# Performance work log

Hardware: AMD Instinct MI355X
Metric: run time of the kernel (lower is better)

Reference implementation:

```python
import jax, jax.numpy as jnp
import numpy as np

D = 128           # embed_dim
NUM_LAYERS = 2
N_CLASSES = 4
OUT_CELL = 64
SPEAKERS = 2
INPUT_DIMS = [768, 74, 35]
B, T = 32, 60


def setup_inputs() -> dict:
    key = jax.random.key(0)
    ks = jax.random.split(key, 24)
    inp = {}
    inp['x0'] = jax.random.normal(ks[0], (B, T, INPUT_DIMS[0]), jnp.float32)
    inp['x1'] = jax.random.normal(ks[1], (B, T, INPUT_DIMS[1]), jnp.float32)
    inp['x2'] = jax.random.normal(ks[2], (B, T, INPUT_DIMS[2]), jnp.float32)
    inp['smask'] = jax.random.normal(ks[3], (B, T, SPEAKERS), jnp.float32)  # argmax -> speaker ids
    # modality projections
    for i, d in enumerate(INPUT_DIMS):
        inp[f'Wp{i}'] = jax.random.normal(ks[4 + i], (d, D), jnp.float32) / np.float32(np.sqrt(d))
        inp[f'bp{i}'] = jnp.zeros((D,), jnp.float32)
    # shared PositionEmbedding (ModuleList([m]*3) shares params)
    inp['freq_emb'] = jax.random.normal(ks[7], (SPEAKERS, D), jnp.float32) * 0.1
    inp['phase_emb'] = jax.random.normal(ks[8], (SPEAKERS, D), jnp.float32)
    # shared QRNNCell (ModuleList([cell]*num_layers) shares params)
    inp['U_x'] = jnp.linalg.qr(jax.random.normal(ks[9], (D, D), jnp.float32))[0]
    inp['U_h'] = jnp.linalg.qr(jax.random.normal(ks[10], (D, D), jnp.float32))[0]
    inp['Lambda'] = jnp.float32(0.5)
    # QMeasurement kernel (real/imag parts of D measurement vectors)
    inp['kernel_r'] = jnp.eye(D, dtype=jnp.float32) + 0.05 * jax.random.normal(ks[11], (D, D), jnp.float32)
    inp['kernel_i'] = 0.05 * jax.random.normal(ks[12], (D, D), jnp.float32)
    # SimpleNet fc_out
    inp['W1'] = jax.random.normal(ks[13], (D, OUT_CELL), jnp.float32) / np.float32(np.sqrt(D))
    inp['b1'] = jnp.zeros((OUT_CELL,), jnp.float32)
    inp['W2'] = jax.random.normal(ks[14], (OUT_CELL, N_CLASSES), jnp.float32) / np.float32(np.sqrt(OUT_CELL))
    inp['b2'] = jnp.zeros((N_CLASSES,), jnp.float32)
    return inp


def _qmn_forward(x0, x1, x2, smask, Wp0, bp0, Wp1, bp1, Wp2, bp2,
                 freq_emb, phase_emb, U_x, U_h, Lambda,
                 kernel_r, kernel_i, W1, b1, W2, b2):
    xs = [x0, x1, x2]
    Ws = [(Wp0, bp0), (Wp1, bp1), (Wp2, bp2)]
    reps = [jax.nn.relu(x @ W + b) for x, (W, b) in zip(xs, Ws)]           # [B,T,D] each
    # mixture weights: softmax over per-modality L2 norms
    norms = jnp.concatenate([jnp.linalg.norm(r, axis=-1, keepdims=True) for r in reps], axis=-1)
    weights = jax.nn.softmax(norms, axis=-1)                               # [B,T,M]
    # shared phase embedding: phase = t * freq[speaker] + phase[speaker]
    ids = jnp.argmax(smask, axis=-1)                                       # [B,T] int
    pos = jnp.arange(T, dtype=jnp.float32)[None, :, None]                  # [1,T,1]
    phase = pos * freq_emb[ids] + phase_emb[ids]                           # [B,T,D]
    cosp, sinp = jnp.cos(phase), jnp.sin(phase)
    # mixed density matrices rho = sum_m w_m |v_m><v_m|
    rho_r = jnp.zeros((B, T, D, D), jnp.float32)
    rho_i = jnp.zeros((B, T, D, D), jnp.float32)
    for m, r in enumerate(reps):
        a = r / jnp.maximum(jnp.linalg.norm(r, axis=-1, keepdims=True), 1e-12)
        pr = a * cosp                                                       # real amplitude
        pi = a * sinp                                                       # imag amplitude
        w = weights[..., m][..., None, None]
        rho_r = rho_r + w * (jnp.einsum('btm,btn->btmn', pr, pr) + jnp.einsum('btm,btn->btmn', pi, pi))
        rho_i = rho_i + w * (jnp.einsum('btm,btn->btmn', pi, pr) - jnp.einsum('btm,btn->btmn', pr, pi))
    # time-major for scan
    sr = jnp.transpose(rho_r, (1, 0, 2, 3))                                # [T,B,D,D]
    si = jnp.transpose(rho_i, (1, 0, 2, 3))

    def cell(h, x):
        hr, hi = h
        xr, xi = x
        Xr = jnp.einsum('mp,bpq,nq->bmn', U_x, xr, U_x)
        Xi = jnp.einsum('mp,bpq,nq->bmn', U_x, xi, U_x)
        Hr = jnp.einsum('mp,bpq,nq->bmn', U_h, hr, U_h)
        Hi = jnp.einsum('mp,bpq,nq->bmn', U_h, hi, U_h)
        nr = Lambda * Hr + (1.0 - Lambda) * Xr
        ni = Lambda * Hi + (1.0 - Lambda) * Xi
        return (nr, ni), (nr, ni)

    h0 = (jnp.broadcast_to(jnp.eye(D, dtype=jnp.float32) / D, (B, D, D)),
          jnp.zeros((B, D, D), jnp.float32))
    for _ in range(NUM_LAYERS):  # same shared cell params each layer
        _, (sr, si) = jax.lax.scan(cell, h0, (sr, si))
    # QMeasurement: p_k = Re(v_k^dag rho v_k), unit-norm complex measurement vectors
    nrm = jnp.sqrt(jnp.sum(kernel_r**2 + kernel_i**2, axis=1, keepdims=True))
    vr = kernel_r / jnp.maximum(nrm, 1e-12)                                # [K,D], K=D
    vi = kernel_i / jnp.maximum(nrm, 1e-12)
    probs = (jnp.einsum('tbmn,km,kn->tbk', sr, vr, vr)
             + jnp.einsum('tbmn,km,kn->tbk', sr, vi, vi)
             - jnp.einsum('tbmn,km,kn->tbk', si, vr, vi)
             + jnp.einsum('tbmn,km,kn->tbk', si, vi, vr))                  # [T,B,D]
    # SimpleNet (dropout = identity at inference)
    hid = jax.nn.relu(probs @ W1 + b1)
    out = jnp.tanh(hid @ W2 + b2)                                          # [T,B,C]
    out = jnp.transpose(out, (1, 0, 2))                                    # [B,T,C]
    return jax.nn.log_softmax(out, axis=2)


def reference(x0, x1, x2, smask, Wp0, bp0, Wp1, bp1, Wp2, bp2,
              freq_emb, phase_emb, U_x, U_h, Lambda,
              kernel_r, kernel_i, W1, b1, W2, b2):
    return _qmn_forward(x0, x1, x2, smask, Wp0, bp0, Wp1, bp1, Wp2, bp2,
                        freq_emb, phase_emb, U_x, U_h, Lambda,
                        kernel_r, kernel_i, W1, b1, W2, b2)
```

## Files before the change

kernel.cpp:

```cpp
#include <hip/hip_runtime.h>


#define DB 32
#define DT 60
#define DD 128
#define BT (DB*DT)
#define SP 136

typedef unsigned short ushort_t;
typedef __attribute__((ext_vector_type(8))) __bf16 bf16x8;
typedef __attribute__((ext_vector_type(8))) unsigned short ushort8_t;
typedef __attribute__((ext_vector_type(4))) float  float4v;

__device__ __forceinline__ float bf2f(ushort_t u){
  union { unsigned int i; float f; } x; x.i = ((unsigned int)u) << 16; return x.f;
}
__device__ __forceinline__ ushort_t f2bf(float f){
  union { float f; unsigned int i; } x; x.f = f;
  unsigned int lsb = (x.i >> 16) & 1u;
  return (ushort_t)((x.i + 0x7FFFu + lsb) >> 16);
}
__device__ __forceinline__ unsigned int f2bfpk(float a, float b){
#if defined(__gfx950__) && __has_builtin(__builtin_amdgcn_cvt_pk_bf16_f32)
  auto v = __builtin_amdgcn_cvt_pk_bf16_f32(a, b);
  unsigned int r; __builtin_memcpy(&r, &v, 4); return r;
#else
  return (unsigned int)f2bf(a) | ((unsigned int)f2bf(b) << 16);
#endif
}
__device__ __forceinline__ void split2(float v, ushort_t& h, ushort_t& l){
  h = f2bf(v); l = f2bf(v - bf2f(h));
}

template<int RT, int CT, bool ALO, bool BLO>
__device__ __forceinline__ void gemm_t(const ushort_t* Ah, const ushort_t* Al,
                                       const ushort_t* Bh, const ushort_t* Bl,
                                       float4v* acc, int row0, int col0, int gma, int q)
{
  for (int ks = 0; ks < 4; ks++){
    int ko = ks*32 + q*8;
    bf16x8 aF[RT], aL[RT], bF[CT], bL[CT];
    #pragma unroll
    for (int R = 0; R < RT; R++){
      int row = row0 + 16*R + gma;
      aF[R] = *(const bf16x8*)&Ah[row*SP + ko];
      if (ALO) aL[R] = *(const bf16x8*)&Al[row*SP + ko];
    }
    #pragma unroll
    for (int C = 0; C < CT; C++){
      int row = col0 + 16*C + gma;
      bF[C] = *(const bf16x8*)&Bh[row*SP + ko];
      if (BLO) bL[C] = *(const bf16x8*)&Bl[row*SP + ko];
    }
    #pragma unroll
    for (int R = 0; R < RT; R++)
      #pragma unroll
      for (int C = 0; C < CT; C++){
        float4v c = acc[R*CT+C];
        c = __builtin_amdgcn_mfma_f32_16x16x32_bf16(aF[R], bF[C], c, 0, 0, 0);
        if (BLO) c = __builtin_amdgcn_mfma_f32_16x16x32_bf16(aF[R], bL[C], c, 0, 0, 0);
        if (ALO) c = __builtin_amdgcn_mfma_f32_16x16x32_bf16(aL[R], bF[C], c, 0, 0, 0);
        acc[R*CT+C] = c;
      }
  }
}

template<int RT, int CT>
__device__ __forceinline__ void emit_t(const float4v* acc, ushort_t* dst, int stride,
                                       int row0, int col0, int gma, int q){
  #pragma unroll
  for (int R = 0; R < RT; R++)
    #pragma unroll
    for (int C = 0; C < CT; C++){
      int c = col0 + 16*C + gma, r0 = row0 + 16*R + 4*q;
      uint2 o;
      o.x = f2bfpk(acc[R*CT+C][0], acc[R*CT+C][1]);
      o.y = f2bfpk(acc[R*CT+C][2], acc[R*CT+C][3]);
      *(uint2*)&dst[(size_t)c*stride + r0] = o;
    }
}
template<int RT, int CT>
__device__ __forceinline__ void emit_split_t(const float4v* acc, ushort_t* dh, ushort_t* dl, int stride,
                                             int row0, int col0, int gma, int q){
  #pragma unroll
  for (int R = 0; R < RT; R++)
    #pragma unroll
    for (int C = 0; C < CT; C++){
      int c = col0 + 16*C + gma, r0 = row0 + 16*R + 4*q;
      ushort4 hh, ll;
      split2(acc[R*CT+C][0], hh.x, ll.x); split2(acc[R*CT+C][1], hh.y, ll.y);
      split2(acc[R*CT+C][2], hh.z, ll.z); split2(acc[R*CT+C][3], hh.w, ll.w);
      *(ushort4*)&dh[(size_t)c*stride + r0] = hh;
      *(ushort4*)&dl[(size_t)c*stride + r0] = ll;
    }
}
template<int NT>
__device__ __forceinline__ void lds_load_mat(ushort_t* dst, const ushort_t* src, int tid){
  for (int i = tid*8; i < 16384; i += NT*8){
    int r = i >> 7, k = i & 127;
    *(ushort8_t*)&dst[r*SP + k] = *(const ushort8_t*)&src[i];
  }
}
template<int NT>
__device__ __forceinline__ void lds_load_rows16(ushort_t* dst, const ushort_t* src, int tid){
  for (int i = tid*8; i < 2048; i += NT*8){
    int r = i >> 7, k = i & 127;
    *(ushort8_t*)&dst[r*SP + k] = *(const ushort8_t*)&src[i];
  }
}
template<int NT>
__device__ __forceinline__ void lds_load_mat2(ushort_t* d0, const ushort_t* s0,
                                              ushort_t* d1, const ushort_t* s1, int tid){
  constexpr int CH = 16384/(NT*8);
  ushort8_t r0[CH], r1[CH];
  #pragma unroll
  for (int c = 0; c < CH; c++) r0[c] = *(const ushort8_t*)&s0[tid*8 + c*NT*8];
  #pragma unroll
  for (int c = 0; c < CH; c++) r1[c] = *(const ushort8_t*)&s1[tid*8 + c*NT*8];
  #pragma unroll
  for (int c = 0; c < CH; c++){
    int i = tid*8 + c*NT*8; int r = i >> 7, k = i & 127;
    *(ushort8_t*)&d0[r*SP + k] = r0[c];
  }
  #pragma unroll
  for (int c = 0; c < CH; c++){
    int i = tid*8 + c*NT*8; int r = i >> 7, k = i & 127;
    *(ushort8_t*)&d1[r*SP + k] = r1[c];
  }
}
template<int NT>
__device__ __forceinline__ void lds_store_mat(ushort_t* dst, const ushort_t* src, int tid){
  for (int i = tid*8; i < 16384; i += NT*8){
    int r = i >> 7, k = i & 127;
    *(ushort8_t*)&dst[i] = *(const ushort8_t*)&src[r*SP + k];
  }
}

__global__ void k_small(const float* Ux, const float* Uh, const float* kr, const float* ki,
                        const float* Wp0, const float* Wp1, const float* Wp2,
                        ushort_t* UxTh, ushort_t* UxTl, ushort_t* UxH, ushort_t* UxL,
                        float* Vr, float* Vi,
                        ushort_t* PpH, ushort_t* PpL, ushort_t* PTh, ushort_t* PTl,
                        ushort_t* WT0h, ushort_t* WT0l, ushort_t* WT1h, ushort_t* WT1l,
                        ushort_t* WT2h, ushort_t* WT2l){
  int blk = blockIdx.x, d = threadIdx.x;
  if (blk < 128){
    int i = blk;
    float v = Ux[i*DD + d];
    ushort_t h, l; split2(v, h, l);
    UxTh[d*DD + i] = h; UxTl[d*DD + i] = l;
  } else if (blk < 256){
    __shared__ float red[DD];
    int k = blk - 128;
    float r = kr[k*DD+d], im = ki[k*DD+d];
    red[d] = r*r + im*im;
    __syncthreads();
    for (int s = 64; s > 0; s >>= 1){ if (d < s) red[d] += red[d+s]; __syncthreads(); }
    float nrm = fmaxf(sqrtf(red[0]), 1e-12f);
    Vr[k*DD+d] = r/nrm; Vi[k*DD+d] = im/nrm;
  } else if (blk < 384){
    int i = blk - 256;
    float v = Uh[i*DD + d];
    ushort_t h, l; split2(v, h, l);
    PpH[i*DD + d] = h;  PpL[i*DD + d] = l;
    PTh[d*DD + i] = h;  PTl[d*DD + i] = l;
  } else {
    int dd2 = blk - 384;
    ushort_t h, l;
    for (int k = d; k < 768; k += 128){
      split2(Wp0[(size_t)k*DD + dd2], h, l);
      WT0h[(size_t)dd2*768 + k] = h; WT0l[(size_t)dd2*768 + k] = l;
    }
    { float v = (d < 74) ? Wp1[(size_t)d*DD + dd2] : 0.f;
      split2(v, h, l); WT1h[dd2*128 + d] = h; WT1l[dd2*128 + d] = l; }
    { float v = (d < 35) ? Wp2[(size_t)d*DD + dd2] : 0.f;
      split2(v, h, l); WT2h[dd2*128 + d] = h; WT2l[dd2*128 + d] = l; }
    { split2(Ux[(size_t)dd2*DD + d], h, l);
      UxH[dd2*DD + d] = h; UxL[dd2*DD + d] = l; }
  }
}

__global__ __launch_bounds__(512,1) void k_proj(
    const float* x0, const float* x1, const float* x2,
    const ushort_t* WT0h, const ushort_t* WT0l,
    const ushort_t* WT1h, const ushort_t* WT1l,
    const ushort_t* WT2h, const ushort_t* WT2l,
    const float* bp0, const float* bp1, const float* bp2,
    float* Reps)
{
  __shared__ ushort_t Ah[128*SP], Al[128*SP], Bh[128*SP], Bl[128*SP];
  int blk = blockIdx.x;
  int tile = blk / 3, m = blk % 3;
  int bt0 = tile*128;
  int tid = threadIdx.x;
  int w = tid >> 6, lane = tid & 63, gma = lane & 15, q = lane >> 4;
  int row0 = 32*(w >> 1), col0 = 64*(w & 1);
  const float* xsrc = (m==0)? x0 : (m==1)? x1 : x2;
  const ushort_t* Wh_ = (m==0)? WT0h : (m==1)? WT1h : WT2h;
  const ushort_t* Wl_ = (m==0)? WT0l : (m==1)? WT1l : WT2l;
  const float* bp = (m==0)? bp0 : (m==1)? bp1 : bp2;
  int KW = (m==0)? 768 : (m==1)? 74 : 35;
  int nch = (m==0)? 6 : 1;
  int KWpad = (m==0)? 768 : 128;
  float4v acc[8];
  #pragma unroll
  for (int i = 0; i < 8; i++) acc[i] = (float4v){0.f,0.f,0.f,0.f};
  for (int ch = 0; ch < nch; ch++){
    if (ch) __syncthreads();
    for (int i = tid*8; i < 16384; i += 4096){
      int r = i >> 7, k = i & 127;
      *(ushort8_t*)&Ah[r*SP + k] = *(const ushort8_t*)&Wh_[(size_t)r*KWpad + ch*128 + k];
      *(ushort8_t*)&Al[r*SP + k] = *(const ushort8_t*)&Wl_[(size_t)r*KWpad + ch*128 + k];
    }
    if (m == 0){
      for (int i = tid*4; i < 16384; i += 2048){
        int r = i >> 7, k = i & 127;
        float4 v = *(const float4*)&xsrc[(size_t)(bt0 + r)*768 + ch*128 + k];
        ushort4 hh, ll;
        split2(v.x, hh.x, ll.x); split2(v.y, hh.y, ll.y);
        split2(v.z, hh.z, ll.z); split2(v.w, hh.w, ll.w);
        *(ushort4*)&Bh[r*SP + k] = hh;
        *(ushort4*)&Bl[r*SP + k] = ll;
      }
    } else {
      for (int i = tid; i < 16384; i += 512){
        int r = i >> 7, k = i & 127;
        float v = (k < KW) ? xsrc[(size_t)(bt0 + r)*KW + k] : 0.f;
        ushort_t h, l; split2(v, h, l);
        Bh[r*SP + k] = h; Bl[r*SP + k] = l;
      }
    }
    __syncthreads();
    gemm_t<2,4,true,true>(Ah, Al, Bh, Bl, acc, row0, col0, gma, q);
  }
  #pragma unroll
  for (int R = 0; R < 2; R++){
    int r0 = row0 + 16*R + 4*q;
    float4 bv = *(const float4*)&bp[r0];
    #pragma unroll
    for (int C = 0; C < 4; C++){
      int c = col0 + 16*C + gma;
      float4v a = acc[R*4+C];
      float4 o;
      o.x = fmaxf(a[0]+bv.x, 0.f); o.y = fmaxf(a[1]+bv.y, 0.f);
      o.z = fmaxf(a[2]+bv.z, 0.f); o.w = fmaxf(a[3]+bv.w, 0.f);
      *(float4*)&Reps[(size_t)(bt0 + c)*384 + m*128 + r0] = o;
    }
  }
}

__global__ __launch_bounds__(128) void k_mix(const float* Reps, const float* smask,
    const float* freq, const float* phem, ushort_t* PsH, ushort_t* PsL, float* Wgt)
{
  __shared__ float part[2][3];
  int bt = blockIdx.x; int t = bt % DT;
  int d = threadIdx.x;
  float r0v = Reps[(size_t)bt*384 + d];
  float r1v = Reps[(size_t)bt*384 + 128 + d];
  float r2v = Reps[(size_t)bt*384 + 256 + d];
  float s0 = r0v*r0v, s1 = r1v*r1v, s2 = r2v*r2v;
  #pragma unroll
  for (int off = 1; off < 64; off <<= 1){
    s0 += __shfl_xor(s0, off, 64);
    s1 += __shfl_xor(s1, off, 64);
    s2 += __shfl_xor(s2, off, 64);
  }
  int wv = d >> 6;
  if ((d & 63) == 0){ part[wv][0] = s0; part[wv][1] = s1; part[wv][2] = s2; }
  __syncthreads();
  float n0 = sqrtf(part[0][0] + part[1][0]);
  float n1 = sqrtf(part[0][1] + part[1][1]);
  float n2 = sqrtf(part[0][2] + part[1][2]);
  float mx = fmaxf(n0, fmaxf(n1, n2));
  float e0 = expf(n0-mx), e1 = expf(n1-mx), e2 = expf(n2-mx);
  float einv = 1.f/(e0+e1+e2);
  if (d < 3) Wgt[bt*3+d] = (d==0?e0:(d==1?e1:e2))*einv;
  float sm0 = smask[bt*2], sm1 = smask[bt*2+1];
  int id = (sm1 > sm0) ? 1 : 0;
  float ph = (float)t * freq[id*DD+d] + phem[id*DD+d];
  float cp = cosf(ph), sp = sinf(ph);
  float a0 = r0v / fmaxf(n0, 1e-12f);
  float a1 = r1v / fmaxf(n1, 1e-12f);
  float a2 = r2v / fmaxf(n2, 1e-12f);
  ushort_t h, l;
  split2(a0*cp, h, l); PsH[((size_t)0*BT + bt)*DD + d] = h; PsL[((size_t)0*BT + bt)*DD + d] = l;
  split2(a1*cp, h, l); PsH[((size_t)1*BT + bt)*DD + d] = h; PsL[((size_t)1*BT + bt)*DD + d] = l;
  split2(a2*cp, h, l); PsH[((size_t)2*BT + bt)*DD + d] = h; PsL[((size_t)2*BT + bt)*DD + d] = l;
  split2(a0*sp, h, l); PsH[((size_t)3*BT + bt)*DD + d] = h; PsL[((size_t)3*BT + bt)*DD + d] = l;
  split2(a1*sp, h, l); PsH[((size_t)4*BT + bt)*DD + d] = h; PsL[((size_t)4*BT + bt)*DD + d] = l;
  split2(a2*sp, h, l); PsH[((size_t)5*BT + bt)*DD + d] = h; PsL[((size_t)5*BT + bt)*DD + d] = l;
}

__global__ __launch_bounds__(512,1) void k_qtrans(const ushort_t* UxH, const ushort_t* UxL,
                                                  const ushort_t* PsH, const ushort_t* PsL,
                                                  ushort_t* Qb){
  __shared__ ushort_t Ah[128*SP], Al[128*SP], Bh[128*SP], Bl[128*SP];
  int blk = blockIdx.x;
  int tid = threadIdx.x;
  int w = tid >> 6, lane = tid & 63, gma = lane & 15, q = lane >> 4;
  int row0 = 32*(w >> 1), col0 = 64*(w & 1);
  size_t rbase = (size_t)blk*128*128;
  lds_load_mat<512>(Ah, UxH, tid);
  lds_load_mat<512>(Al, UxL, tid);
  lds_load_mat<512>(Bh, PsH + rbase, tid);
  lds_load_mat<512>(Bl, PsL + rbase, tid);
  __syncthreads();
  float4v acc[8];
  #pragma unroll
  for (int i = 0; i < 8; i++) acc[i] = (float4v){0.f,0.f,0.f,0.f};
  gemm_t<2,4,true,true>(Ah, Al, Bh, Bl, acc, row0, col0, gma, q);
  emit_t<2,4>(acc, Qb + rbase, 128, row0, col0, gma, q);
}

__global__ __launch_bounds__(256,2) void k_pow2v2(ushort_t* PpH, ushort_t* PpL,
                                                  ushort_t* PTh, ushort_t* PTl, int s){
  __shared__ ushort_t Ah[128*SP], Al[128*SP], Bh[16*SP], Bl[16*SP];
  int blk = blockIdx.x;
  int which = blk >> 3, sl = blk & 7;
  size_t src = (size_t)(s-1)*16384, dst = (size_t)s*16384;
  int tid = threadIdx.x;
  int w = tid >> 6, lane = tid & 63, gma = lane & 15, q = lane >> 4;
  int row0 = 32*w;
  int gcol0 = sl*16;
  const ushort_t *A_h, *A_l, *B_h, *B_l; ushort_t *D_h, *D_l;
  if (which == 0){ A_h = PTh+src; A_l = PTl+src; B_h = PpH+src; B_l = PpL+src;
                   D_h = PpH+dst; D_l = PpL+dst; }
  else           { A_h = PpH+src; A_l = PpL+src; B_h = PTh+src; B_l = PTl+src;
                   D_h = PTh+dst; D_l = PTl+dst; }
  lds_load_mat<256>(Ah, A_h, tid);
  lds_load_mat<256>(Al, A_l, tid);
  lds_load_rows16<256>(Bh, B_h + (size_t)gcol0*128, tid);
  lds_load_rows16<256>(Bl, B_l + (size_t)gcol0*128, tid);
  __syncthreads();
  float4v acc[2];
  acc[0] = (float4v){0.f,0.f,0.f,0.f};
  acc[1] = (float4v){0.f,0.f,0.f,0.f};
  gemm_t<2,1,true,true>(Ah, Al, Bh, Bl, acc, row0, 0, gma, q);
  emit_split_t<2,1>(acc, D_h, D_l, 128, row0, gcol0, gma, q);
}

__global__ __launch_bounds__(512,1) void k_gchain(const ushort_t* PpH, const ushort_t* PpL,
                                                  const ushort_t* PTh, const ushort_t* PTl,
                                                  ushort_t* GTh, ushort_t* GTl){
  __shared__ ushort_t Ah[128*SP], Al[128*SP], Bh[128*SP], Bl[128*SP];
  int t = blockIdx.x;
  int tid = threadIdx.x;
  int w = tid >> 6, lane = tid & 63, gma = lane & 15, q = lane >> 4;
  int row0 = 32*(w >> 1), col0 = 64*(w & 1);
  size_t gslot = (size_t)t * 16384;
  if (t == 0){
    for (int i = tid*4; i < 16384; i += 2048){
      int r = i >> 7, k = i & 127;
      ushort4 zz; zz.x = zz.y = zz.z = zz.w = 0;
      *(ushort4*)&GTl[gslot + i] = zz;
      ushort4 oh;
      oh.x = (r == (k+0)) ? (ushort_t)0x3F80 : (ushort_t)0;
      oh.y = (r == (k+1)) ? (ushort_t)0x3F80 : (ushort_t)0;
      oh.z = (r == (k+2)) ? (ushort_t)0x3F80 : (ushort_t)0;
      oh.w = (r == (k+3)) ? (ushort_t)0x3F80 : (ushort_t)0;
      *(ushort4*)&GTh[gslot + i] = oh;
    }
    return;
  }
  int b0 = __ffs(t) - 1;
  int rem = t & ~(1 << b0);
  if (rem == 0){
    size_t ps = (size_t)b0 * 16384;
    for (int i = tid*4; i < 16384; i += 2048){
      *(ushort4*)&GTh[gslot + i] = *(const ushort4*)&PTh[ps + i];
      *(ushort4*)&GTl[gslot + i] = *(const ushort4*)&PTl[ps + i];
    }
    return;
  }
  lds_load_mat<512>(Ah, PpH + (size_t)b0*16384, tid);
  lds_load_mat<512>(Al, PpL + (size_t)b0*16384, tid);
  while (rem){
    int k = __ffs(rem) - 1;
    rem &= ~(1 << k);
    lds_load_mat<512>(Bh, PTh + (size_t)k*16384, tid);
    lds_load_mat<512>(Bl, PTl + (size_t)k*16384, tid);
    __syncthreads();
    float4v acc[8];
    #pragma unroll
    for (int i = 0; i < 8; i++) acc[i] = (float4v){0.f,0.f,0.f,0.f};
    if (rem){
      gemm_t<2,4,true,true>(Bh, Bl, Ah, Al, acc, row0, col0, gma, q);
      __syncthreads();
      emit_split_t<2,4>(acc, Ah, Al, SP, row0, col0, gma, q);
      __syncthreads();
    } else {
      gemm_t<2,4,true,true>(Ah, Al, Bh, Bl, acc, row0, col0, gma, q);
      emit_split_t<2,4>(acc, GTh + gslot, GTl + gslot, 128, row0, col0, gma, q);
    }
  }
}

__global__ __launch_bounds__(256,1) void k_precompMW(const ushort_t* GTh, const ushort_t* GTl,
                                                     const ushort_t* UxTh, const ushort_t* UxTl,
                                                     const float* Vr, const float* Vi,
                                                     ushort_t* Mh, ushort_t* Wh){
  __shared__ ushort_t Bh[128*SP], Bl[128*SP], Ah[128*SP], Al[128*SP];
  int blk = blockIdx.x;
  int tid = threadIdx.x;
  int w = tid >> 6, lane = tid & 63, gma = lane & 15, q = lane >> 4;
  int row0 = 64*(w >> 1), col0 = 64*(w & 1);
  if (blk < 60){
    int t = blk;
    lds_load_mat<256>(Bh, GTh + (size_t)t*16384, tid);
    lds_load_mat<256>(Bl, GTl + (size_t)t*16384, tid);
    lds_load_mat<256>(Ah, UxTh, tid);
    lds_load_mat<256>(Al, UxTl, tid);
    __syncthreads();
    float4v acc[16];
    #pragma unroll
    for (int i = 0; i < 16; i++) acc[i] = (float4v){0.f,0.f,0.f,0.f};
    gemm_t<4,4,true,true>(Ah, Al, Bh, Bl, acc, row0, col0, gma, q);
    __syncthreads();
    emit_split_t<4,4>(acc, Ah, Al, SP, row0, col0, gma, q);
    __syncthreads();
    #pragma unroll
    for (int i = 0; i < 16; i++) acc[i] = (float4v){0.f,0.f,0.f,0.f};
    gemm_t<4,4,true,true>(Bh, Bl, Ah, Al, acc, row0, col0, gma, q);
    #pragma unroll
    for (int R = 0; R < 4; R++)
      #pragma unroll
      for (int C = 0; C < 4; C++){
        int c = col0 + 16*C + gma, r0 = row0 + 16*R + 4*q;
        uint2 o;
        o.x = f2bfpk(acc[R*4+C][0], acc[R*4+C][1]);
        o.y = f2bfpk(acc[R*4+C][2], acc[R*4+C][3]);
        *(uint2*)&Mh[(size_t)t*16384 + c*128 + r0] = o;
      }
  } else {
    int bx = blk - 60;
    int t = bx >> 1, which = bx & 1;
    lds_load_mat<256>(Ah, GTh + (size_t)t*16384, tid);
    lds_load_mat<256>(Al, GTl + (size_t)t*16384, tid);
    const float* V = which ? Vi : Vr;
    for (int i = tid; i < 16384; i += 256){
      int r = i >> 7, k = i & 127;
      ushort_t h, l; split2(V[i], h, l);
      Bh[r*SP + k] = h; Bl[r*SP + k] = l;
    }
    __syncthreads();
    float4v acc[16];
    #pragma unroll
    for (int i = 0; i < 16; i++) acc[i] = (float4v){0.f,0.f,0.f,0.f};
    gemm_t<4,4,true,true>(Ah, Al, Bh, Bl, acc, row0, col0, gma, q);
    #pragma unroll
    for (int R = 0; R < 4; R++)
      #pragma unroll
      for (int C = 0; C < 4; C++){
        int c = col0 + 16*C + gma, r0 = row0 + 16*R + 4*q;
        uint2 o;
        o.x = f2bfpk(acc[R*4+C][0], acc[R*4+C][1]);
        o.y = f2bfpk(acc[R*4+C][2], acc[R*4+C][3]);
        *(uint2*)&Wh[(size_t)bx*16384 + c*128 + r0] = o;
      }
  }
}

__global__ __launch_bounds__(512,1) void k_vtrans(const ushort_t* GTh, const ushort_t* Qb, ushort_t* At){
  __shared__ ushort_t Ah[128*SP];
  __shared__ ushort_t Bs[192*SP];
  int t = blockIdx.x;
  int tid = threadIdx.x;
  int w = tid >> 6, lane = tid & 63, gma = lane & 15, q = lane >> 4;
  int row0 = (w & 3)*32, col0 = (w >> 2)*96;
  lds_load_mat<512>(Ah, GTh + (size_t)t*16384, tid);
  for (int i = tid*8; i < 192*128; i += 4096){
    int m = i >> 7, k = i & 127;
    int j = m >> 5, b = m & 31;
    *(ushort8_t*)&Bs[m*SP + k] =
      *(const ushort8_t*)&Qb[((size_t)(j*BT) + b*DT + t)*DD + k];
  }
  __syncthreads();
  float4v acc[12];
  #pragma unroll
  for (int i = 0; i < 12; i++) acc[i] = (float4v){0.f,0.f,0.f,0.f};
  gemm_t<2,6,false,false>(Ah, Ah, Bs, Bs, acc, row0, col0, gma, q);
  emit_t<2,6>(acc, At + (size_t)t*24576, 128, row0, col0, gma, q);
}

__global__ __launch_bounds__(256) void k_zbuild(ushort_t* S, const ushort_t* At,
                                                const float* Wgt, const float* lamp){
  __shared__ ushort_t As[6*DD];
  __shared__ float wl[3];
  int blk = blockIdx.x;
  int b = blk >> 4, slab = blk & 15;
  int tid = threadIdx.x;
  int r = slab*8 + (tid >> 5);
  int c0 = (tid & 31)*4;
  float lam = lamp[0];
  float z0=0.f, z1=0.f, z2=0.f, z3=0.f;
  size_t off = (size_t)slab*1024 + tid*4;
  for (int t = 0; t < DT; t++){
    __syncthreads();
    if (tid < 192){
      int i = tid*4;
      int jj = i >> 7, n = i & 127;
      *(ushort4*)&As[i] = *(const ushort4*)&At[(size_t)t*24576 + (jj*32 + b)*128 + n];
    }
    if (tid < 3) wl[tid] = Wgt[(b*DT + t)*3 + tid];
    __syncthreads();
    float ar[6];
    #pragma unroll
    for (int jj = 0; jj < 6; jj++) ar[jj] = bf2f(As[jj*128 + r]);
    float cb[6];
    cb[0] = wl[0]*(ar[0]+ar[3]); cb[1] = wl[1]*(ar[1]+ar[4]); cb[2] = wl[2]*(ar[2]+ar[5]);
    cb[3] = wl[0]*(ar[3]-ar[0]); cb[4] = wl[1]*(ar[4]-ar[1]); cb[5] = wl[2]*(ar[5]-ar[2]);
    float y0=0.f, y1=0.f, y2=0.f, y3=0.f;
    #pragma unroll
    for (int jj = 0; jj < 6; jj++){
      ushort4 a4 = *(const ushort4*)&As[jj*128 + c0];
      float w_ = cb[jj];
      y0 += w_*bf2f(a4.x); y1 += w_*bf2f(a4.y);
      y2 += w_*bf2f(a4.z); y3 += w_*bf2f(a4.w);
    }
    z0 = lam*z0 + y0; z1 = lam*z1 + y1;
    z2 = lam*z2 + y2; z3 = lam*z3 + y3;
    uint2 o; o.x = f2bfpk(z0, z1); o.y = f2bfpk(z2, z3);
    *(uint2*)&S[((size_t)(t*32 + b))*16384 + off] = o;
  }
}

__global__ __launch_bounds__(512,4) void k_conjmid(ushort_t* S, const ushort_t* Mh,
                                                   const float* lamp){
  __shared__ ushort_t Bh[128*SP], Zs[128*SP];
  int blk = blockIdx.x;
  int t = blk >> 5;
  size_t slot = (size_t)blk * 16384;
  int tid = threadIdx.x;
  int w = tid >> 6, lane = tid & 63, gma = lane & 15, q = lane >> 4;
  int row0 = 32*(w >> 1), col0 = 64*(w & 1);
  lds_load_mat2<512>(Zs, S + slot, Bh, Mh + (size_t)t*16384, tid);
  __syncthreads();
  float lam = lamp[0];
  float oml = 1.f - lam;
  float ct = powf(lam, (float)(t+1)) / 128.f;
  float4v acc[8];
  #pragma unroll
  for (int i = 0; i < 8; i++) acc[i] = (float4v){0.f,0.f,0.f,0.f};
  gemm_t<2,4,false,false>(Zs, Zs, Bh, Bh, acc, row0, col0, gma, q);
  __syncthreads();
  emit_t<2,4>(acc, Zs, SP, row0, col0, gma, q);
  __syncthreads();
  #pragma unroll
  for (int i = 0; i < 8; i++) acc[i] = (float4v){0.f,0.f,0.f,0.f};
  gemm_t<2,4,false,false>(Zs, Zs, Bh, Bh, acc, row0, col0, gma, q);
  __syncthreads();
  #pragma unroll
  for (int R = 0; R < 2; R++)
    #pragma unroll
    for (int C = 0; C < 4; C++){
      int c = col0 + 16*C + gma, r0 = row0 + 16*R + 4*q;
      float v0 = oml*acc[R*4+C][0] + ((c == r0+0) ? ct : 0.f);
      float v1 = oml*acc[R*4+C][1] + ((c == r0+1) ? ct : 0.f);
      float v2 = oml*acc[R*4+C][2] + ((c == r0+2) ? ct : 0.f);
      float v3 = oml*acc[R*4+C][3] + ((c == r0+3) ? ct : 0.f);
      uint2 o; o.x = f2bfpk(v0, v1); o.y = f2bfpk(v2, v3);
      *(uint2*)&Zs[(size_t)c*SP + r0] = o;
    }
  __syncthreads();
  lds_store_mat<512>(S + slot, Zs, tid);
}

__device__ __forceinline__ void prefix_phase(ushort8_t& buf, bool doload,
                                             const ushort_t* Snext, ushort_t* Scur,
                                             float* a, float lam){
  ushort8_t u = buf;
  if (doload) buf = *(const ushort8_t*)Snext;
  #pragma unroll
  for (int i = 0; i < 8; i++) a[i] = lam*a[i] + bf2f(u[i]);
  uint4 o;
  o.x = f2bfpk(a[0],a[1]); o.y = f2bfpk(a[2],a[3]);
  o.z = f2bfpk(a[4],a[5]); o.w = f2bfpk(a[6],a[7]);
  *(uint4*)Scur = o;
}
__global__ __launch_bounds__(128) void k_prefix(ushort_t* S, const float* lamp){
  int blk = blockIdx.x;
  int chain = blk >> 4, slab = blk & 15;
  int tid = threadIdx.x;
  size_t off = (size_t)slab*1024 + tid*8;
  float lam = lamp[0];
  float a[8];
  #pragma unroll
  for (int i = 0; i < 8; i++) a[i] = 0.f;
  size_t addr = (size_t)chain*16384 + off;
  const size_t step = (size_t)32*16384;
  ushort8_t b0 = *(const ushort8_t*)&S[addr];
  ushort8_t b1 = *(const ushort8_t*)&S[addr + step];
  ushort8_t b2 = *(const ushort8_t*)&S[addr + 2*step];
  ushort8_t b3 = *(const ushort8_t*)&S[addr + 3*step];
  for (int t = 0; t < DT; t += 4){
    prefix_phase(b0, t+4 < DT, &S[addr + 4*step], &S[addr], a, lam); addr += step;
    prefix_phase(b1, t+5 < DT, &S[addr + 4*step], &S[addr], a, lam); addr += step;
    prefix_phase(b2, t+6 < DT, &S[addr + 4*step], &S[addr], a, lam); addr += step;
    prefix_phase(b3, t+7 < DT, &S[addr + 4*step], &S[addr], a, lam); addr += step;
  }
}

__global__ __launch_bounds__(512,2) void k_meas(const ushort_t* S, const ushort_t* Wh,
                                                const float* lamp, float* Probs){
  __shared__ ushort_t Vs[128*SP], Cs[128*SP];
  __shared__ float Pd[64];
  int raw = blockIdx.x;
  int tb = (raw & 7) | ((raw >> 4) << 3);
  int h  = (raw >> 3) & 1;
  int t = tb >> 5;
  int tid = threadIdx.x;
  int w = tid >> 6, lane = tid & 63, gma = lane & 15, q = lane >> 4;
  int row0 = 16*(w >> 1);
  int col0 = 64*(w & 1);
  size_t slot = (size_t)tb * 16384;
  size_t wbase = (size_t)(t*2) * 16384;
  ushort8_t creg[4], vreg[4];
  #pragma unroll
  for (int c = 0; c < 4; c++)
    creg[c] = *(const ushort8_t*)&S[slot + tid*8 + c*4096];
  #pragma unroll
  for (int c = 0; c < 4; c++){
    int i = tid*8 + c*4096;
    int r = i >> 7, k = i & 127;
    size_t gsrc = wbase + ((r < 64) ? 0 : 16384) + (size_t)(64*h + (r & 63))*128 + k;
    vreg[c] = *(const ushort8_t*)&Wh[gsrc];
  }
  if (tid < 64) Pd[tid] = 0.f;
  #pragma unroll
  for (int c = 0; c < 4; c++){
    int i = tid*8 + c*4096;
    int r = i >> 7, k = i & 127;
    *(ushort8_t*)&Cs[r*SP + k] = creg[c];
  }
  #pragma unroll
  for (int c = 0; c < 4; c++){
    int i = tid*8 + c*4096;
    int r = i >> 7, k = i & 127;
    *(ushort8_t*)&Vs[r*SP + k] = vreg[c];
  }
  __syncthreads();
  float4v acc[8];
  #pragma unroll
  for (int i = 0; i < 8; i++) acc[i] = (float4v){0.f,0.f,0.f,0.f};
  #pragma unroll
  for (int ks = 0; ks < 4; ks++){
    int ko = ks*32 + q*8;
    bf16x8 aF0 = *(const bf16x8*)&Vs[(row0 + gma)*SP + ko];
    bf16x8 aF1 = *(const bf16x8*)&Vs[(row0 + 64 + gma)*SP + ko];
    bf16x8 bF[4];
    #pragma unroll
    for (int C = 0; C < 4; C++)
      bF[C] = *(const bf16x8*)&Cs[(col0 + 16*C + gma)*SP + ko];
    #pragma unroll
    for (int C = 0; C < 4; C++){
      acc[C]   = __builtin_amdgcn_mfma_f32_16x16x32_bf16(aF0, bF[C], acc[C],   0, 0, 0);
      acc[4+C] = __builtin_amdgcn_mfma_f32_16x16x32_bf16(aF1, bF[C], acc[4+C], 0, 0, 0);
    }
  }
  #pragma unroll
  for (int j = 0; j < 4; j++){
    int kr = row0 + 4*q + j;
    float s = 0.f;
    #pragma unroll
    for (int C = 0; C < 4; C++){
      int m = col0 + 16*C + gma;
      float w0 = bf2f(Vs[kr*SP + m]);
      float w1 = bf2f(Vs[(kr + 64)*SP + m]);
      s += acc[C][j]*(w0 + w1) + acc[4+C][j]*(w1 - w0);
    }
    #pragma unroll
    for (int off = 1; off < 16; off <<= 1)
      s += __shfl_xor(s, off, 64);
    if (gma == 0) atomicAdd(&Pd[kr], s);
  }
  __syncthreads();
  if (tid < 64){
    float lam = lamp[0];
    float ct = powf(lam, (float)(t+1)) / 128.f;
    Probs[(size_t)tb*DD + 64*h + tid] = (1.f - lam)*Pd[tid] + ct;
  }
}

__global__ __launch_bounds__(64) void k_head(const float* Probs, const float* W1, const float* b1,
                        const float* W2, const float* b2, float* out)
{
  __shared__ float ps[DD];
  __shared__ float hid[64];
  __shared__ float ov[4];
  int tb = blockIdx.x;
  int tid = threadIdx.x;
  ps[tid] = Probs[(size_t)tb*DD + tid];
  ps[tid+64] = Probs[(size_t)tb*DD + 64 + tid];
  __syncthreads();
  float acc = b1[tid];
  for (int dd = 0; dd < DD; dd++) acc += ps[dd]*W1[dd*64 + tid];
  hid[tid] = fmaxf(acc, 0.f);
  __syncthreads();
  if (tid < 4){
    float o = b2[tid];
    for (int j = 0; j < 64; j++) o += hid[j]*W2[j*4 + tid];
    ov[tid] = tanhf(o);
  }
  __syncthreads();
  if (tid == 0){
    float m = fmaxf(fmaxf(ov[0],ov[1]), fmaxf(ov[2],ov[3]));
    float lse = logf(expf(ov[0]-m)+expf(ov[1]-m)+expf(ov[2]-m)+expf(ov[3]-m));
    int t = tb >> 5, b = tb & 31;
    float* o = out + ((size_t)(b*DT + t))*4;
    o[0] = ov[0]-m-lse; o[1] = ov[1]-m-lse;
    o[2] = ov[2]-m-lse; o[3] = ov[3]-m-lse;
  }
}

extern "C" void kernel_launch(void* const* d_in, const int* in_sizes, int n_in,
                              void* d_out, int out_size, void* d_ws, size_t ws_size,
                              hipStream_t stream)
{
  const float* x0    = (const float*)d_in[0];
  const float* x1    = (const float*)d_in[1];
  const float* x2    = (const float*)d_in[2];
  const float* smask = (const float*)d_in[3];
  const float* Wp0   = (const float*)d_in[4];
  const float* bp0   = (const float*)d_in[5];
  const float* Wp1   = (const float*)d_in[6];
  const float* bp1   = (const float*)d_in[7];
  const float* Wp2   = (const float*)d_in[8];
  const float* bp2   = (const float*)d_in[9];
  const float* freq  = (const float*)d_in[10];
  const float* phem  = (const float*)d_in[11];
  const float* Ux    = (const float*)d_in[12];
  const float* Uh    = (const float*)d_in[13];
  const float* lamp  = (const float*)d_in[14];
  const float* kr    = (const float*)d_in[15];
  const float* ki    = (const float*)d_in[16];
  const float* W1    = (const float*)d_in[17];
  const float* b1    = (const float*)d_in[18];
  const float* W2    = (const float*)d_in[19];
  const float* b2    = (const float*)d_in[20];

  char* ws = (char*)d_ws;
  auto alignup = [](size_t x){ return (x + 255) & ~(size_t)255; };
  size_t off = 0;
  ushort_t* S   = (ushort_t*)(ws + off); off = alignup(off + (size_t)1920*16384*sizeof(ushort_t));
  ushort_t* Qb  = (ushort_t*)(ws + off); off = alignup(off + (size_t)6*BT*DD*sizeof(ushort_t));
  float* Reps   = (float*)(ws + off);    off = alignup(off + (size_t)BT*384*sizeof(float));
  ushort_t* PsH = (ushort_t*)(ws + off); off = alignup(off + (size_t)6*BT*DD*sizeof(ushort_t));
  ushort_t* PsL = (ushort_t*)(ws + off); off = alignup(off + (size_t)6*BT*DD*sizeof(ushort_t));
  float* Wgt    = (float*)(ws + off);    off = alignup(off + (size_t)BT*3*sizeof(float));
  float* Vr     = (float*)(ws + off);    off = alignup(off + (size_t)DD*DD*sizeof(float));
  float* Vi     = (float*)(ws + off);    off = alignup(off + (size_t)DD*DD*sizeof(float));
  ushort_t* UxTh = (ushort_t*)(ws + off); off = alignup(off + (size_t)DD*DD*sizeof(ushort_t));
  ushort_t* UxTl = (ushort_t*)(ws + off); off = alignup(off + (size_t)DD*DD*sizeof(ushort_t));
  ushort_t* UxH = (ushort_t*)(ws + off); off = alignup(off + (size_t)DD*DD*sizeof(ushort_t));
  ushort_t* UxL = (ushort_t*)(ws + off); off = alignup(off + (size_t)DD*DD*sizeof(ushort_t));
  float* Probs  = (float*)(ws + off);    off = alignup(off + (size_t)BT*DD*sizeof(float));
  ushort_t* PpH = (ushort_t*)(ws + off); off = alignup(off + (size_t)6*16384*sizeof(ushort_t));
  ushort_t* PpL = (ushort_t*)(ws + off); off = alignup(off + (size_t)6*16384*sizeof(ushort_t));
  ushort_t* PTh = (ushort_t*)(ws + off); off = alignup(off + (size_t)6*16384*sizeof(ushort_t));
  ushort_t* PTl = (ushort_t*)(ws + off); off = alignup(off + (size_t)6*16384*sizeof(ushort_t));
  ushort_t* Mh  = (ushort_t*)(ws + off); off = alignup(off + (size_t)60*16384*sizeof(ushort_t));
  ushort_t* Wmh = (ushort_t*)(ws + off); off = alignup(off + (size_t)120*16384*sizeof(ushort_t));
  ushort_t* GTh = (ushort_t*)(ws + off); off = alignup(off + (size_t)60*16384*sizeof(ushort_t));
  ushort_t* GTl = (ushort_t*)(ws + off); off = alignup(off + (size_t)60*16384*sizeof(ushort_t));
  ushort_t* At  = (ushort_t*)(ws + off); off = alignup(off + (size_t)60*24576*sizeof(ushort_t));
  ushort_t* WT0h = (ushort_t*)(ws + off); off = alignup(off + (size_t)128*768*sizeof(ushort_t));
  ushort_t* WT0l = (ushort_t*)(ws + off); off = alignup(off + (size_t)128*768*sizeof(ushort_t));
  ushort_t* WT1h = (ushort_t*)(ws + off); off = alignup(off + (size_t)128*128*sizeof(ushort_t));
  ushort_t* WT1l = (ushort_t*)(ws + off); off = alignup(off + (size_t)128*128*sizeof(ushort_t));
  ushort_t* WT2h = (ushort_t*)(ws + off); off = alignup(off + (size_t)128*128*sizeof(ushort_t));
  ushort_t* WT2l = (ushort_t*)(ws + off); off = alignup(off + (size_t)128*128*sizeof(ushort_t));
  (void)ws_size; (void)in_sizes; (void)n_in; (void)out_size;

  k_small<<<512, 128, 0, stream>>>(Ux, Uh, kr, ki, Wp0, Wp1, Wp2,
                                   UxTh, UxTl, UxH, UxL, Vr, Vi,
                                   PpH, PpL, PTh, PTl,
                                   WT0h, WT0l, WT1h, WT1l, WT2h, WT2l);
  k_proj<<<45, 512, 0, stream>>>(x0, x1, x2, WT0h, WT0l, WT1h, WT1l, WT2h, WT2l,
                                 bp0, bp1, bp2, Reps);
  k_mix<<<BT, 128, 0, stream>>>(Reps, smask, freq, phem, PsH, PsL, Wgt);
  k_qtrans<<<90, 512, 0, stream>>>(UxH, UxL, PsH, PsL, Qb);
  for (int s = 1; s <= 5; s++)
    k_pow2v2<<<16, 256, 0, stream>>>(PpH, PpL, PTh, PTl, s);
  k_gchain<<<60, 512, 0, stream>>>(PpH, PpL, PTh, PTl, GTh, GTl);
  k_precompMW<<<180, 256, 0, stream>>>(GTh, GTl, UxTh, UxTl, Vr, Vi, Mh, Wmh);
  k_vtrans<<<60, 512, 0, stream>>>(GTh, Qb, At);
  k_zbuild<<<512, 256, 0, stream>>>(S, At, Wgt, lamp);
  k_conjmid<<<1920, 512, 0, stream>>>(S, Mh, lamp);
  k_prefix<<<512, 128, 0, stream>>>(S, lamp);
  k_meas<<<3840, 512, 0, stream>>>(S, Wmh, lamp, Probs);
  k_head<<<BT, 64, 0, stream>>>(Probs, W1, b1, W2, b2, (float*)d_out);
}
```

Before: 361.2 us.

## Split projection GEMM along K and pre-convert inputs to bf16 hi/lo

A new k_xconv kernel converts x0/x1/x2 to split bf16 hi/lo arrays once. k_proj is relaunched with 120 blocks instead of 45: the 768-wide modality is split into 6 K-chunks that each write partial sums. k_mix then reduces the six partials and applies bias and ReLU. The aim is to fill more CUs in the projection stage, at the cost of an extra launch and extra global traffic for the converted inputs and the partial sums.

Result: faster. 332.6 us (-7.9%).

```diff
diff --git a/kernel.cpp b/kernel.cpp
--- a/kernel.cpp
+++ b/kernel.cpp
@@ -180,82 +180,102 @@
   }
 }
 
+__global__ __launch_bounds__(128) void k_xconv(const float* x0, const float* x1, const float* x2,
+    ushort_t* X0h, ushort_t* X0l, ushort_t* X1h, ushort_t* X1l, ushort_t* X2h, ushort_t* X2l){
+  int bt = blockIdx.x, d = threadIdx.x;
+  ushort_t h, l;
+  const float* r0 = x0 + (size_t)bt*768;
+  #pragma unroll
+  for (int j = 0; j < 6; j++){
+    split2(r0[j*128 + d], h, l);
+    X0h[(size_t)bt*768 + j*128 + d] = h;
+    X0l[(size_t)bt*768 + j*128 + d] = l;
+  }
+  float v1 = (d < 74) ? x1[(size_t)bt*74 + d] : 0.f;
+  split2(v1, h, l);
+  X1h[(size_t)bt*128 + d] = h; X1l[(size_t)bt*128 + d] = l;
+  float v2 = (d < 35) ? x2[(size_t)bt*35 + d] : 0.f;
+  split2(v2, h, l);
+  X2h[(size_t)bt*128 + d] = h; X2l[(size_t)bt*128 + d] = l;
+}
+
 __global__ __launch_bounds__(512,1) void k_proj(
-    const float* x0, const float* x1, const float* x2,
-    const ushort_t* WT0h, const ushort_t* WT0l,
-    const ushort_t* WT1h, const ushort_t* WT1l,
+    const ushort_t* X0h, const ushort_t* X0l, const ushort_t* X1h, const ushort_t* X1l,
+    const ushort_t* X2h, const ushort_t* X2l,
+    const ushort_t* WT0h, const ushort_t* WT0l, const ushort_t* WT1h, const ushort_t* WT1l,
     const ushort_t* WT2h, const ushort_t* WT2l,
-    const float* bp0, const float* bp1, const float* bp2,
-    float* Reps)
+    const float* bp1, const float* bp2,
+    float* Rpart, float* Reps)
 {
   __shared__ ushort_t Ah[128*SP], Al[128*SP], Bh[128*SP], Bl[128*SP];
   int blk = blockIdx.x;
-  int tile = blk / 3, m = blk % 3;
+  int m, tile, ch;
+  if (blk < 90){ m = 0; tile = blk/6; ch = blk%6; }
+  else if (blk < 105){ m = 1; tile = blk-90; ch = 0; }
+  else { m = 2; tile = blk-105; ch = 0; }
   int bt0 = tile*128;
   int tid = threadIdx.x;
   int w = tid >> 6, lane = tid & 63, gma = lane & 15, q = lane >> 4;
   int row0 = 32*(w >> 1), col0 = 64*(w & 1);
-  const float* xsrc = (m==0)? x0 : (m==1)? x1 : x2;
   const ushort_t* Wh_ = (m==0)? WT0h : (m==1)? WT1h : WT2h;
   const ushort_t* Wl_ = (m==0)? WT0l : (m==1)? WT1l : WT2l;
-  const float* bp = (m==0)? bp0 : (m==1)? bp1 : bp2;
-  int KW = (m==0)? 768 : (m==1)? 74 : 35;
-  int nch = (m==0)? 6 : 1;
-  int KWpad = (m==0)? 768 : 128;
+  const ushort_t* Xh_ = (m==0)? X0h : (m==1)? X1h : X2h;
+  const ushort_t* Xl_ = (m==0)? X0l : (m==1)? X1l : X2l;
+  int KX = (m==0)? 768 : 128;
+  for (int i = tid*8; i < 16384; i += 4096){
+    int r = i >> 7, k = i & 127;
+    *(ushort8_t*)&Ah[r*SP + k] = *(const ushort8_t*)&Wh_[(size_t)r*KX + ch*128 + k];
+    *(ushort8_t*)&Al[r*SP + k] = *(const ushort8_t*)&Wl_[(size_t)r*KX + ch*128 + k];
+    *(ushort8_t*)&Bh[r*SP + k] = *(const ushort8_t*)&Xh_[(size_t)(bt0+r)*KX + ch*128 + k];
+    *(ushort8_t*)&Bl[r*SP + k] = *(const ushort8_t*)&Xl_[(size_t)(bt0+r)*KX + ch*128 + k];
+  }
+  __syncthreads();
   float4v acc[8];
   #pragma unroll
   for (int i = 0; i < 8; i++) acc[i] = (float4v){0.f,0.f,0.f,0.f};
-  for (int ch = 0; ch < nch; ch++){
-    if (ch) __syncthreads();
-    for (int i = tid*8; i < 16384; i += 4096){
-      int r = i >> 7, k = i & 127;
-      *(ushort8_t*)&Ah[r*SP + k] = *(const ushort8_t*)&Wh_[(size_t)r*KWpad + ch*128 + k];
-      *(ushort8_t*)&Al[r*SP + k] = *(const ushort8_t*)&Wl_[(size_t)r*KWpad + ch*128 + k];
-    }
-    if (m == 0){
-      for (int i = tid*4; i < 16384; i += 2048){
-        int r = i >> 7, k = i & 127;
-        float4 v = *(const float4*)&xsrc[(size_t)(bt0 + r)*768 + ch*128 + k];
-        ushort4 hh, ll;
-        split2(v.x, hh.x, ll.x); split2(v.y, hh.y, ll.y);
-        split2(v.z, hh.z, ll.z); split2(v.w, hh.w, ll.w);
-        *(ushort4*)&Bh[r*SP + k] = hh;
-        *(ushort4*)&Bl[r*SP + k] = ll;
+  gemm_t<2,4,true,true>(Ah, Al, Bh, Bl, acc, row0, col0, gma, q);
+  if (m == 0){
+    #pragma unroll
+    for (int R = 0; R < 2; R++)
+      #pragma unroll
+      for (int C = 0; C < 4; C++){
+        int c = col0 + 16*C + gma, r0 = row0 + 16*R + 4*q;
+        float4 o;
+        o.x = acc[R*4+C][0]; o.y = acc[R*4+C][1];
+        o.z = acc[R*4+C][2]; o.w = acc[R*4+C][3];
+        *(float4*)&Rpart[((size_t)ch*BT + bt0 + c)*128 + r0] = o;
       }
-    } else {
-      for (int i = tid; i < 16384; i += 512){
-        int r = i >> 7, k = i & 127;
-        float v = (k < KW) ? xsrc[(size_t)(bt0 + r)*KW + k] : 0.f;
-        ushort_t h, l; split2(v, h, l);
-        Bh[r*SP + k] = h; Bl[r*SP + k] = l;
+  } else {
+    const float* bp = (m==1)? bp1 : bp2;
+    #pragma unroll
+    for (int R = 0; R < 2; R++){
+      int r0 = row0 + 16*R + 4*q;
+      float4 bv = *(const float4*)&bp[r0];
+      #pragma unroll
+      for (int C = 0; C < 4; C++){
+        int c = col0 + 16*C + gma;
+        float4v a = acc[R*4+C];
+        float4 o;
+        o.x = fmaxf(a[0]+bv.x, 0.f); o.y = fmaxf(a[1]+bv.y, 0.f);
+        o.z = fmaxf(a[2]+bv.z, 0.f); o.w = fmaxf(a[3]+bv.w, 0.f);
+        *(float4*)&Reps[(size_t)(bt0 + c)*384 + m*128 + r0] = o;
       }
     }
-    __syncthreads();
-    gemm_t<2,4,true,true>(Ah, Al, Bh, Bl, acc, row0, col0, gma, q);
-  }
-  #pragma unroll
-  for (int R = 0; R < 2; R++){
-    int r0 = row0 + 16*R + 4*q;
-    float4 bv = *(const float4*)&bp[r0];
-    #pragma unroll
-    for (int C = 0; C < 4; C++){
-      int c = col0 + 16*C + gma;
-      float4v a = acc[R*4+C];
-      float4 o;
-      o.x = fmaxf(a[0]+bv.x, 0.f); o.y = fmaxf(a[1]+bv.y, 0.f);
-      o.z = fmaxf(a[2]+bv.z, 0.f); o.w = fmaxf(a[3]+bv.w, 0.f);
-      *(float4*)&Reps[(size_t)(bt0 + c)*384 + m*128 + r0] = o;
-    }
-  }
-}
-
-__global__ __launch_bounds__(128) void k_mix(const float* Reps, const float* smask,
+  }
+}
+
+__global__ __launch_bounds__(128) void k_mix(const float* Rpart, const float* Reps,
+    const float* bp0, const float* smask,
     const float* freq, const float* phem, ushort_t* PsH, ushort_t* PsL, float* Wgt)
 {
   __shared__ float part[2][3];
   int bt = blockIdx.x; int t = bt % DT;
   int d = threadIdx.x;
-  float r0v = Reps[(size_t)bt*384 + d];
+  float r0v = bp0[d];
+  #pragma unroll
+  for (int ch = 0; ch < 6; ch++)
+    r0v += Rpart[((size_t)ch*BT + bt)*128 + d];
+  r0v = fmaxf(r0v, 0.f);
   float r1v = Reps[(size_t)bt*384 + 128 + d];
   float r2v = Reps[(size_t)bt*384 + 256 + d];
   float s0 = r0v*r0v, s1 = r1v*r1v, s2 = r2v*r2v;
@@ -743,9 +763,16 @@
   size_t off = 0;
   ushort_t* S   = (ushort_t*)(ws + off); off = alignup(off + (size_t)1920*16384*sizeof(ushort_t));
   ushort_t* Qb  = (ushort_t*)(ws + off); off = alignup(off + (size_t)6*BT*DD*sizeof(ushort_t));
+  float* Rpart  = (float*)(ws + off);    off = alignup(off + (size_t)6*BT*DD*sizeof(float));
   float* Reps   = (float*)(ws + off);    off = alignup(off + (size_t)BT*384*sizeof(float));
   ushort_t* PsH = (ushort_t*)(ws + off); off = alignup(off + (size_t)6*BT*DD*sizeof(ushort_t));
   ushort_t* PsL = (ushort_t*)(ws + off); off = alignup(off + (size_t)6*BT*DD*sizeof(ushort_t));
+  ushort_t* X0h = (ushort_t*)(ws + off); off = alignup(off + (size_t)BT*768*sizeof(ushort_t));
+  ushort_t* X0l = (ushort_t*)(ws + off); off = alignup(off + (size_t)BT*768*sizeof(ushort_t));
+  ushort_t* X1h = (ushort_t*)(ws + off); off = alignup(off + (size_t)BT*128*sizeof(ushort_t));
+  ushort_t* X1l = (ushort_t*)(ws + off); off = alignup(off + (size_t)BT*128*sizeof(ushort_t));
+  ushort_t* X2h = (ushort_t*)(ws + off); off = alignup(off + (size_t)BT*128*sizeof(ushort_t));
+  ushort_t* X2l = (ushort_t*)(ws + off); off = alignup(off + (size_t)BT*128*sizeof(ushort_t));
   float* Wgt    = (float*)(ws + off);    off = alignup(off + (size_t)BT*3*sizeof(float));
   float* Vr     = (float*)(ws + off);    off = alignup(off + (size_t)DD*DD*sizeof(float));
   float* Vi     = (float*)(ws + off);    off = alignup(off + (size_t)DD*DD*sizeof(float));
@@ -775,9 +802,11 @@
                                    UxTh, UxTl, UxH, UxL, Vr, Vi,
                                    PpH, PpL, PTh, PTl,
                                    WT0h, WT0l, WT1h, WT1l, WT2h, WT2l);
-  k_proj<<<45, 512, 0, stream>>>(x0, x1, x2, WT0h, WT0l, WT1h, WT1l, WT2h, WT2l,
-                                 bp0, bp1, bp2, Reps);
-  k_mix<<<BT, 128, 0, stream>>>(Reps, smask, freq, phem, PsH, PsL, Wgt);
+  k_xconv<<<BT, 128, 0, stream>>>(x0, x1, x2, X0h, X0l, X1h, X1l, X2h, X2l);
+  k_proj<<<120, 512, 0, stream>>>(X0h, X0l, X1h, X1l, X2h, X2l,
+                                  WT0h, WT0l, WT1h, WT1l, WT2h, WT2l,
+                                  bp1, bp2, Rpart, Reps);
+  k_mix<<<BT, 128, 0, stream>>>(Rpart, Reps, bp0, smask, freq, phem, PsH, PsL, Wgt);
   k_qtrans<<<90, 512, 0, stream>>>(UxH, UxL, PsH, PsL, Qb);
   for (int s = 1; s <= 5; s++)
     k_pow2v2<<<16, 256, 0, stream>>>(PpH, PpL, PTh, PTl, s);
```
